# Kernel optimization log

Measured on AMD Instinct MI355X. Metric: run time of the kernel, lower is better.

The kernel has to match this reference:

```python
import jax, jax.numpy as jnp
import numpy as np

N, T, D, M = 16, 4096, 256, 512


def setup_inputs() -> dict:
    key = jax.random.key(0)
    k1, k2 = jax.random.split(key)
    x = jax.random.normal(k1, (N, T, D), dtype=jnp.float32)
    # codebook initialized like the module: uniform(-1/M, 1/M) then row-normalized
    init_bound = 1.0 / M
    emb = jax.random.uniform(k2, (M, D), dtype=jnp.float32, minval=-init_bound, maxval=init_bound)
    emb = emb / (jnp.linalg.norm(emb, axis=1, keepdims=True) + 1e-4)
    return {"x": x, "embedding": emb}


def reference(x, embedding):
    sg = jax.lax.stop_gradient
    # L2_distance: distances computed against the row-normalized codebook,
    # but the gather uses the raw (unnormalized) codebook.
    emb_norm = embedding / (jnp.linalg.norm(embedding, axis=1, keepdims=True) + 1e-4)
    x_flat = sg(x).reshape(-1, D)  # (N*T, D), detached in torch
    distances = (jnp.sum(emb_norm ** 2, axis=1)[None, :]
                 + jnp.sum(x_flat ** 2, axis=1, keepdims=True)
                 - 2.0 * (x_flat @ emb_norm.T))  # (N*T, M)
    indices = jnp.argmin(distances, axis=-1)  # (N*T,)
    encodings = jax.nn.one_hot(indices, M, dtype=jnp.float32)  # (N*T, M)
    quantized = embedding[indices].reshape(x.shape)  # (N, T, D)

    commitment_loss = jnp.mean((sg(x) - quantized) ** 2)
    quantized_ = x + sg(quantized - x)           # straight-through
    quantized_ = (quantized_ + quantized) / 2.0  # averaged with raw-grad path

    avg_probs = jnp.mean(encodings, axis=0)  # (M,)
    perplexity = jnp.exp(-jnp.sum(avg_probs * jnp.log(avg_probs + 1e-10)))
    return quantized_, commitment_loss, perplexity
```

## Files before the change

### kernel.cpp

```cpp
#include <hip/hip_runtime.h>
#include <hip/hip_bf16.h>


typedef _Float16 half8_t __attribute__((ext_vector_type(8)));
typedef _Float16 half4_t __attribute__((ext_vector_type(4)));
typedef float f32x4 __attribute__((ext_vector_type(4)));

static constexpr int kRows = 65536;
static constexpr int kD = 256;
static constexpr int kM = 512;
static constexpr int kBM = 128;

typedef const unsigned int __attribute__((address_space(1)))* gas_t;
typedef unsigned int __attribute__((address_space(3)))* las_t;

__global__ void vq_prep(const float* __restrict__ emb, _Float16* __restrict__ swz,
                        float* __restrict__ bias, unsigned int* __restrict__ hist,
                        float* __restrict__ loss) {
    const int j = blockIdx.x;
    const int lane = threadIdx.x;
    float4 v = ((const float4*)(emb + j * kD))[lane];
    float ss = v.x * v.x + v.y * v.y + v.z * v.z + v.w * v.w;
    #pragma unroll
    for (int off = 32; off > 0; off >>= 1) ss += __shfl_xor(ss, off);
    const float scale = 1.0f / (sqrtf(ss) + 1e-4f);
    if (lane == 0) bias[j] = 0.5f * ss * scale * scale;
    half4_t h;
    h[0] = (_Float16)(v.x * scale);
    h[1] = (_Float16)(v.y * scale);
    h[2] = (_Float16)(v.z * scale);
    h[3] = (_Float16)(v.w * scale);
    const int k0 = lane * 4;
    const int ko = k0 >> 5;
    const int qd = (k0 >> 3) & 3;
    const int jj = k0 & 7;
    const int off_h = (j >> 4) * 4096 + ko * 512 + (qd * 16 + (j & 15)) * 8 + jj;
    *(half4_t*)(swz + off_h) = h;
    if (j == 0) {
        for (int b = lane; b < kM; b += 64) hist[b] = 0u;
        if (lane == 0) loss[0] = 0.0f;
    }
}

__global__ __launch_bounds__(512, 4) void vq_main(
    const float* __restrict__ x, const float* __restrict__ emb,
    const _Float16* __restrict__ bswz, const float* __restrict__ bias,
    unsigned int* __restrict__ hist, float* __restrict__ loss_accum,
    float* __restrict__ out) {
    __shared__ _Float16 bb[128 * kD];
    __shared__ float lbias[kM];
    __shared__ unsigned int lhist[kM];
    __shared__ int lidx[kBM];
    __shared__ float lred[8];

    const int t = threadIdx.x;
    const int row0 = blockIdx.x * kBM;
    const int wave = t >> 6;
    const int lane = t & 63;
    const int qd = lane >> 4;
    const int ln = lane & 15;
    const int m0 = wave * 16;

    lhist[t] = 0u;
    lbias[t] = bias[t];

    half8_t a[8];
    {
        const float* xr = x + (size_t)(row0 + m0 + ln) * kD + qd * 8;
        #pragma unroll
        for (int ko = 0; ko < 8; ++ko) {
            const float4 v0 = *(const float4*)(xr + ko * 32);
            const float4 v1 = *(const float4*)(xr + ko * 32 + 4);
            half8_t h;
            h[0] = (_Float16)v0.x; h[1] = (_Float16)v0.y;
            h[2] = (_Float16)v0.z; h[3] = (_Float16)v0.w;
            h[4] = (_Float16)v1.x; h[5] = (_Float16)v1.y;
            h[6] = (_Float16)v1.z; h[7] = (_Float16)v1.w;
            a[ko] = h;
        }
    }

    float bv[4] = {-1e30f, -1e30f, -1e30f, -1e30f};
    int bi[4] = {0, 0, 0, 0};
    #pragma unroll 1
    for (int s = 0; s < 4; ++s) {
        __syncthreads();
        {
            const _Float16* src = bswz + (size_t)s * 32768 + t * 8;
            _Float16* dst = bb + t * 8;
            #pragma unroll
            for (int i = 0; i < 8; ++i)
                __builtin_amdgcn_global_load_lds((gas_t)(const void*)(src + i * 4096),
                                                 (las_t)(void*)(dst + i * 4096), 16, 0, 0);
        }
        __syncthreads();
        #pragma unroll
        for (int sub = 0; sub < 8; ++sub) {
            const int c = s * 128 + sub * 16 + ln;
            const float bbias = lbias[c];
            f32x4 acc = {-bbias, -bbias, -bbias, -bbias};
            const half8_t* bp = (const half8_t*)bb + sub * 512 + lane;
            #pragma unroll
            for (int ko = 0; ko < 8; ++ko)
                acc = __builtin_amdgcn_mfma_f32_16x16x32_f16(a[ko], bp[ko * 64], acc, 0, 0, 0);
            #pragma unroll
            for (int r = 0; r < 4; ++r)
                if (acc[r] > bv[r]) { bv[r] = acc[r]; bi[r] = c; }
        }
    }

    #pragma unroll
    for (int r = 0; r < 4; ++r) {
        #pragma unroll
        for (int off = 1; off < 16; off <<= 1) {
            const float ov = __shfl_xor(bv[r], off);
            const int oi = __shfl_xor(bi[r], off);
            if (ov > bv[r] || (ov == bv[r] && oi < bi[r])) { bv[r] = ov; bi[r] = oi; }
        }
        if (ln == 0) {
            const int row = m0 + qd * 4 + r;
            lidx[row] = bi[r];
            atomicAdd(&lhist[bi[r]], 1u);
        }
    }
    __syncthreads();

    float lsum = 0.0f;
    {
        const float* xg = x + (size_t)row0 * kD;
        float* og = out + (size_t)row0 * kD;
        #pragma unroll
        for (int i = 0; i < 16; ++i) {
            const int g = t * 4 + i * 2048;
            const int r = g >> 8;
            const float4 xv = *(const float4*)(xg + g);
            const int idx = lidx[r];
            const float4 q = *(const float4*)(emb + (size_t)idx * kD + (g & 255));
            const float d0 = xv.x - q.x, d1 = xv.y - q.y, d2 = xv.z - q.z, d3 = xv.w - q.w;
            lsum += d0 * d0 + d1 * d1 + d2 * d2 + d3 * d3;
            float4 o;
            o.x = ((xv.x + (q.x - xv.x)) + q.x) * 0.5f;
            o.y = ((xv.y + (q.y - xv.y)) + q.y) * 0.5f;
            o.z = ((xv.z + (q.z - xv.z)) + q.z) * 0.5f;
            o.w = ((xv.w + (q.w - xv.w)) + q.w) * 0.5f;
            *(float4*)&og[g] = o;
        }
    }
    #pragma unroll
    for (int off = 32; off > 0; off >>= 1) lsum += __shfl_xor(lsum, off);
    if (lane == 0) lred[wave] = lsum;
    __syncthreads();
    if (t == 0) {
        float bs = 0.f;
        #pragma unroll
        for (int w = 0; w < 8; ++w) bs += lred[w];
        atomicAdd(loss_accum, bs);
    }

    const unsigned int h0 = lhist[t];
    if (h0) atomicAdd(&hist[t], h0);
}

__global__ void vq_final(const unsigned int* __restrict__ hist,
                         const float* __restrict__ loss_accum,
                         float* __restrict__ out) {
    const int t = threadIdx.x;
    __shared__ float sr[4];
    float s = 0.0f;
    for (int b = t; b < kM; b += 256) {
        const float p = (float)hist[b] * (1.0f / 65536.0f);
        s += p * logf(p + 1e-10f);
    }
    #pragma unroll
    for (int off = 32; off > 0; off >>= 1) s += __shfl_xor(s, off);
    if ((t & 63) == 0) sr[t >> 6] = s;
    __syncthreads();
    if (t == 0) {
        const float tot = sr[0] + sr[1] + sr[2] + sr[3];
        out[16777217] = expf(-tot);
        out[16777216] = loss_accum[0] * (1.0f / 16777216.0f);
    }
}

extern "C" void kernel_launch(void* const* d_in, const int* in_sizes, int n_in,
                              void* d_out, int out_size, void* d_ws, size_t ws_size,
                              hipStream_t stream) {
    const float* x = (const float*)d_in[0];
    const float* emb = (const float*)d_in[1];
    char* ws = (char*)d_ws;
    _Float16* bswz = (_Float16*)ws;
    float* bias = (float*)(ws + 262144);
    unsigned int* hist = (unsigned int*)(ws + 262144 + 2048);
    float* loss = (float*)(ws + 262144 + 4096);
    float* out = (float*)d_out;

    vq_prep<<<kM, 64, 0, stream>>>(emb, bswz, bias, hist, loss);
    vq_main<<<kRows / kBM, 512, 0, stream>>>(x, emb, bswz, bias, hist, loss, out);
    vq_final<<<1, 256, 0, stream>>>(hist, loss, out);
}
```

Measured before the change: 138.6 us.

## Shrink blocks to 64 rows with two 16-row MFMA tiles per wave

Blocks drop from 8 waves over 128 rows to 2 waves over 64 rows. Each wave now computes two 16-row tiles that share every LDS B-fragment read, and the codebook is staged in 8 chunks of 64 codes (32 KB LDS) instead of 4 chunks of 128. The aim is to halve LDS B traffic per MFMA and raise occupancy through a smaller LDS footprint and more blocks. The cost is that each block reloads the full codebook for only 64 rows, doubling total codebook L2 traffic, and there are more barriers per block with fewer waves to hide them.

```diff
diff --git a/kernel.cpp b/kernel.cpp
--- a/kernel.cpp
+++ b/kernel.cpp
@@ -9,7 +9,7 @@
 static constexpr int kRows = 65536;
 static constexpr int kD = 256;
 static constexpr int kM = 512;
-static constexpr int kBM = 128;
+static constexpr int kBM = 64;
 
 typedef const unsigned int __attribute__((address_space(1)))* gas_t;
 typedef unsigned int __attribute__((address_space(3)))* las_t;
@@ -42,16 +42,16 @@
     }
 }
 
-__global__ __launch_bounds__(512, 4) void vq_main(
+__global__ __launch_bounds__(128, 2) void vq_main(
     const float* __restrict__ x, const float* __restrict__ emb,
     const _Float16* __restrict__ bswz, const float* __restrict__ bias,
     unsigned int* __restrict__ hist, float* __restrict__ loss_accum,
     float* __restrict__ out) {
-    __shared__ _Float16 bb[128 * kD];
+    __shared__ _Float16 bb[64 * kD];
     __shared__ float lbias[kM];
     __shared__ unsigned int lhist[kM];
     __shared__ int lidx[kBM];
-    __shared__ float lred[8];
+    __shared__ float lred[2];
 
     const int t = threadIdx.x;
     const int row0 = blockIdx.x * kBM;
@@ -59,14 +59,14 @@
     const int lane = t & 63;
     const int qd = lane >> 4;
     const int ln = lane & 15;
-    const int m0 = wave * 16;
-
-    lhist[t] = 0u;
-    lbias[t] = bias[t];
-
-    half8_t a[8];
-    {
-        const float* xr = x + (size_t)(row0 + m0 + ln) * kD + qd * 8;
+
+    #pragma unroll
+    for (int b = t; b < kM; b += 128) { lhist[b] = 0u; lbias[b] = bias[b]; }
+
+    half8_t a[2][8];
+    #pragma unroll
+    for (int s = 0; s < 2; ++s) {
+        const float* xr = x + (size_t)(row0 + wave * 32 + s * 16 + ln) * kD + qd * 8;
         #pragma unroll
         for (int ko = 0; ko < 8; ++ko) {
             const float4 v0 = *(const float4*)(xr + ko * 32);
@@ -76,51 +76,60 @@
             h[2] = (_Float16)v0.z; h[3] = (_Float16)v0.w;
             h[4] = (_Float16)v1.x; h[5] = (_Float16)v1.y;
             h[6] = (_Float16)v1.z; h[7] = (_Float16)v1.w;
-            a[ko] = h;
-        }
-    }
-
-    float bv[4] = {-1e30f, -1e30f, -1e30f, -1e30f};
-    int bi[4] = {0, 0, 0, 0};
+            a[s][ko] = h;
+        }
+    }
+
+    float bv[2][4] = {{-1e30f, -1e30f, -1e30f, -1e30f}, {-1e30f, -1e30f, -1e30f, -1e30f}};
+    int bi[2][4] = {{0, 0, 0, 0}, {0, 0, 0, 0}};
     #pragma unroll 1
-    for (int s = 0; s < 4; ++s) {
+    for (int st = 0; st < 8; ++st) {
         __syncthreads();
         {
-            const _Float16* src = bswz + (size_t)s * 32768 + t * 8;
-            _Float16* dst = bb + t * 8;
-            #pragma unroll
-            for (int i = 0; i < 8; ++i)
-                __builtin_amdgcn_global_load_lds((gas_t)(const void*)(src + i * 4096),
-                                                 (las_t)(void*)(dst + i * 4096), 16, 0, 0);
+            const _Float16* src = bswz + (size_t)st * 16384 + wave * 512 + lane * 8;
+            _Float16* dst = bb + wave * 512 + lane * 8;
+            #pragma unroll
+            for (int i = 0; i < 16; ++i)
+                __builtin_amdgcn_global_load_lds((gas_t)(const void*)(src + i * 1024),
+                                                 (las_t)(void*)(dst + i * 1024), 16, 0, 0);
         }
         __syncthreads();
         #pragma unroll
-        for (int sub = 0; sub < 8; ++sub) {
-            const int c = s * 128 + sub * 16 + ln;
+        for (int sg = 0; sg < 4; ++sg) {
+            const int c = st * 64 + sg * 16 + ln;
             const float bbias = lbias[c];
-            f32x4 acc = {-bbias, -bbias, -bbias, -bbias};
-            const half8_t* bp = (const half8_t*)bb + sub * 512 + lane;
-            #pragma unroll
-            for (int ko = 0; ko < 8; ++ko)
-                acc = __builtin_amdgcn_mfma_f32_16x16x32_f16(a[ko], bp[ko * 64], acc, 0, 0, 0);
-            #pragma unroll
-            for (int r = 0; r < 4; ++r)
-                if (acc[r] > bv[r]) { bv[r] = acc[r]; bi[r] = c; }
-        }
-    }
-
-    #pragma unroll
-    for (int r = 0; r < 4; ++r) {
+            f32x4 acc0 = {-bbias, -bbias, -bbias, -bbias};
+            f32x4 acc1 = {-bbias, -bbias, -bbias, -bbias};
+            const half8_t* bp = (const half8_t*)bb + sg * 512 + lane;
+            #pragma unroll
+            for (int ko = 0; ko < 8; ++ko) {
+                const half8_t bf = bp[ko * 64];
+                acc0 = __builtin_amdgcn_mfma_f32_16x16x32_f16(a[0][ko], bf, acc0, 0, 0, 0);
+                acc1 = __builtin_amdgcn_mfma_f32_16x16x32_f16(a[1][ko], bf, acc1, 0, 0, 0);
+            }
+            #pragma unroll
+            for (int r = 0; r < 4; ++r) {
+                if (acc0[r] > bv[0][r]) { bv[0][r] = acc0[r]; bi[0][r] = c; }
+                if (acc1[r] > bv[1][r]) { bv[1][r] = acc1[r]; bi[1][r] = c; }
+            }
+        }
+    }
+
+    #pragma unroll
+    for (int s = 0; s < 2; ++s) {
         #pragma unroll
-        for (int off = 1; off < 16; off <<= 1) {
-            const float ov = __shfl_xor(bv[r], off);
-            const int oi = __shfl_xor(bi[r], off);
-            if (ov > bv[r] || (ov == bv[r] && oi < bi[r])) { bv[r] = ov; bi[r] = oi; }
-        }
-        if (ln == 0) {
-            const int row = m0 + qd * 4 + r;
-            lidx[row] = bi[r];
-            atomicAdd(&lhist[bi[r]], 1u);
+        for (int r = 0; r < 4; ++r) {
+            #pragma unroll
+            for (int off = 1; off < 16; off <<= 1) {
+                const float ov = __shfl_xor(bv[s][r], off);
+                const int oi = __shfl_xor(bi[s][r], off);
+                if (ov > bv[s][r] || (ov == bv[s][r] && oi < bi[s][r])) { bv[s][r] = ov; bi[s][r] = oi; }
+            }
+            if (ln == 0) {
+                const int row = wave * 32 + s * 16 + qd * 4 + r;
+                lidx[row] = bi[s][r];
+                atomicAdd(&lhist[bi[s][r]], 1u);
+            }
         }
     }
     __syncthreads();
@@ -129,9 +138,9 @@
     {
         const float* xg = x + (size_t)row0 * kD;
         float* og = out + (size_t)row0 * kD;
-        #pragma unroll
-        for (int i = 0; i < 16; ++i) {
-            const int g = t * 4 + i * 2048;
+        #pragma unroll 8
+        for (int i = 0; i < 32; ++i) {
+            const int g = t * 4 + i * 512;
             const int r = g >> 8;
             const float4 xv = *(const float4*)(xg + g);
             const int idx = lidx[r];
@@ -150,15 +159,13 @@
     for (int off = 32; off > 0; off >>= 1) lsum += __shfl_xor(lsum, off);
     if (lane == 0) lred[wave] = lsum;
     __syncthreads();
-    if (t == 0) {
-        float bs = 0.f;
-        #pragma unroll
-        for (int w = 0; w < 8; ++w) bs += lred[w];
-        atomicAdd(loss_accum, bs);
-    }
-
-    const unsigned int h0 = lhist[t];
-    if (h0) atomicAdd(&hist[t], h0);
+    if (t == 0) atomicAdd(loss_accum, lred[0] + lred[1]);
+
+    #pragma unroll
+    for (int b = t; b < kM; b += 128) {
+        const unsigned int h = lhist[b];
+        if (h) atomicAdd(&hist[b], h);
+    }
 }
 
 __global__ void vq_final(const unsigned int* __restrict__ hist,
@@ -195,6 +202,6 @@
     float* out = (float*)d_out;
 
     vq_prep<<<kM, 64, 0, stream>>>(emb, bswz, bias, hist, loss);
-    vq_main<<<kRows / kBM, 512, 0, stream>>>(x, emb, bswz, bias, hist, loss, out);
+    vq_main<<<kRows / kBM, 128, 0, stream>>>(x, emb, bswz, bias, hist, loss, out);
     vq_final<<<1, 256, 0, stream>>>(hist, loss, out);
 }
```

Measured after the change: 147.8 us. 6.7% more time.
